# Optimization experiments

Hardware: AMD Instinct MI355X
Metric: run time of the kernel (lower is better)

Reference implementation:

```python
import jax, jax.numpy as jnp
import numpy as np

SHIFT = 1  # fixed shift_direction (module draws +/-1 at random; we pin +1)

def setup_inputs() -> dict:
    key = jax.random.key(0)
    kx, kw = jax.random.split(key)
    x = jax.random.normal(kx, (1024, 256, 7, 7), dtype=jnp.float32)
    W = jax.random.normal(kw, (128, 3, 3, 512), dtype=jnp.float32)
    return {"x": x, "W": W}

def _fwd(x, W):
    B = x.shape[0]
    t = x.reshape(B, 256, 7, 7)
    # unfold((3,1), padding=(1,0)) along H: t[b,c,k,h,w] = x_pad[b,c,h+k-1,w]
    xp = jnp.pad(t, ((0, 0), (0, 0), (1, 1), (0, 0)))
    t = jnp.stack([xp[:, :, k:k + 7, :] for k in range(3)], axis=2)  # (B,256,3,7,7)
    t = t.reshape(B, 2, 128, 3, 7, 7).transpose(0, 2, 3, 4, 1, 5)   # (B,128,3,7,2,7)
    t = t.reshape(B, 128, 3, 14, 7)
    t = jnp.roll(t, SHIFT, axis=3)
    t = t.reshape(B, 128, 3, 7, 2, 7).sum(axis=4)                   # (B,128,3,7,7)
    t = t.transpose(0, 1, 3, 2, 4)                                  # (B,128,7,3,7)
    t = jnp.roll(t, SHIFT, axis=4)
    # second unfold((3,1), padding=(1,0)) along W dim: gather 3 shifted slices
    tp = jnp.pad(t, ((0, 0), (0, 0), (0, 0), (0, 0), (1, 1)))
    t3 = jnp.stack([tp[..., k2:k2 + 7] for k2 in range(3)], axis=-1)  # (B,128,7,3,7,3) = (m,l,n,j,o,k)
    out = jnp.einsum('mlnjok,ljki->mnoi', t3, W)                     # (B,7,7,512)
    return out.transpose(0, 3, 1, 2)                                 # (B,512,7,7)

def reference(x, W):
    return _fwd(x, W)
```

## Files before the change

kernel.cpp:

```cpp
#include <hip/hip_runtime.h>

typedef __attribute__((ext_vector_type(8)))  __bf16 bvec8;
typedef __attribute__((ext_vector_type(4)))  __bf16 bvec4;
typedef __attribute__((ext_vector_type(16))) float  fvec16;
typedef __attribute__((ext_vector_type(8)))  short  svec8;

__global__ __launch_bounds__(256) void pack_w(const float* __restrict__ W,
                                              __bf16* __restrict__ Wp) {
    int u = blockIdx.x * 256 + threadIdx.x;
    if (u >= 73728) return;
    int lane = u & 63;
    int f    = (u >> 6) & 3;
    int wd   = (u >> 8) & 7;
    int t    = u >> 11;
    int am = f & 1, h = f >> 1;
    int i  = (wd << 6) + (am << 5) + (lane & 31);
    int K0 = ((2 * t + h) << 4) + ((lane >> 5) << 3);
    bvec8 o;
#pragma unroll
    for (int e = 0; e < 8; ++e) {
        int K  = K0 + e;
        int jk = K >> 7;
        int l  = K & 127;
        int j  = (jk * 11) >> 5;
        int k  = jk - 3 * j;
        o[e] = (__bf16)W[((l * 9 + j * 3 + k) << 9) + i];
    }
    *(bvec8*)&Wp[(size_t)u * 8] = o;
}

__global__ __launch_bounds__(512, 2) void conv_mfma(
    const float* __restrict__ x, const __bf16* __restrict__ Wp,
    float* __restrict__ out)
{
    __shared__ __align__(16) char smem[65024];
    __bf16* xs = (__bf16*)smem;
    __bf16* ys = (__bf16*)(smem + 25088);

    const int tid  = threadIdx.x;
    const int lane = tid & 63;
    const int l31  = lane & 31;
    const int ls5  = lane >> 5;
    const int wd   = tid >> 6;
    const int b0   = blockIdx.x * 2;

    const float* xb  = x + (size_t)b0 * 12544;
    const char*  WpB = (const char*)Wp;
    const int wbase  = wd * 4096 + lane * 16;

    bvec8 aE[2][2], aO[2][2];
#pragma unroll
    for (int am = 0; am < 2; ++am)
#pragma unroll
        for (int h = 0; h < 2; ++h) {
            aE[am][h] = *(const bvec8*)(WpB + wbase + ((h * 2 + am) << 10));
            aO[am][h] = *(const bvec8*)(WpB + 32768 + wbase + ((h * 2 + am) << 10));
        }

    for (int bb = 0; bb < 2; ++bb) {
        for (int it = 0; it < 7; ++it) {
            int e4 = it * 512 + tid;
            if (e4 < 3136) {
                const float4 v = ((const float4*)(xb + bb * 12544))[e4];
                bvec4 pk = { (__bf16)v.x, (__bf16)v.y, (__bf16)v.z, (__bf16)v.w };
                *(bvec4*)&xs[e4 * 4] = pk;
            }
        }
        __syncthreads();
        for (int it = 0; it < 3; ++it) {
            int up = it * 512 + tid;
            if (up < 1248) {
                int row  = up >> 4;
                int useg = up & 15;
                int l0   = useg * 8;
                bvec8 ov;
                if (row == 77) {
                    ov = __builtin_bit_cast(bvec8, (svec8)0);
                } else if (row < 63) {
                    int t = row / 7, w = row - t * 7;
                    int tb = t + 5; if (tb >= 7) tb -= 7;
                    int cB = tb * 7 + w;
                    bool mA = (t >= 1) && (t <= 7);
                    int cA = mA ? (t - 1) * 7 + w : 0;
#pragma unroll
                    for (int d = 0; d < 8; ++d) {
                        float fa = mA ? (float)xs[(l0 + d) * 49 + cA] : 0.f;
                        float fb = (float)xs[(128 + l0 + d) * 49 + cB];
                        ov[d] = (__bf16)(fa + fb);
                    }
                } else if (row < 70) {
                    int w = row - 63;
#pragma unroll
                    for (int d = 0; d < 8; ++d) ov[d] = xs[(l0 + d) * 49 + w];
                } else {
                    int w = row - 70;
#pragma unroll
                    for (int d = 0; d < 8; ++d) ov[d] = xs[(l0 + d) * 49 + 7 + w];
                }
                *(bvec8*)&ys[((bb * 78 + row) << 7) + ((useg ^ (row & 15)) << 3)] = ov;
            }
        }
        __syncthreads();
    }

    int nq[2], oo[2];
#pragma unroll
    for (int sn = 0; sn < 2; ++sn) {
        int s = sn * 32 + l31;
        int sc = (s < 49) ? s : 48;
        nq[sn] = sc / 7;
        oo[sn] = sc - nq[sn] * 7;
    }

    fvec16 acc[2][2][2];
#pragma unroll
    for (int am = 0; am < 2; ++am)
#pragma unroll
        for (int sn = 0; sn < 2; ++sn)
#pragma unroll
            for (int bb = 0; bb < 2; ++bb)
#pragma unroll
                for (int r = 0; r < 16; ++r) acc[am][sn][bb][r] = 0.f;

#define GEO(JK, ROWE, RX) {                                                   \
        int j_ = ((JK) * 11) >> 5; int k_ = (JK) - 3 * j_;                    \
        _Pragma("unroll")                                                     \
        for (int sn_ = 0; sn_ < 2; ++sn_) {                                   \
            int tw_ = oo[sn_] + k_ + 5; int w_ = tw_ >= 7 ? tw_ - 7 : tw_;    \
            int row_ = (nq[sn_] + j_) * 7 + w_;                               \
            if (nq[sn_] == 1 && j_ == 0) row_ = 63 + w_;                      \
            if (nq[sn_] == 0 && j_ == 2) row_ = 70 + w_;                      \
            if ((k_ == 0 && oo[sn_] == 0) || (k_ == 2 && oo[sn_] == 6))       \
                row_ = 77;                                                    \
            ROWE[sn_] = row_ << 7; RX[sn_] = row_ & 15; } }

#define READF(DST, P, ROWE, RX) {                                             \
        _Pragma("unroll")                                                     \
        for (int sn_ = 0; sn_ < 2; ++sn_)                                     \
        _Pragma("unroll")                                                     \
        for (int h_ = 0; h_ < 2; ++h_) {                                      \
            int u_ = ((P) * 4 + h_ * 2 + ls5) ^ RX[sn_];                      \
            DST[sn_][0][h_] = *(const bvec8*)&ys[ROWE[sn_] + (u_ << 3)];      \
            DST[sn_][1][h_] = *(const bvec8*)&ys[9984 + ROWE[sn_] + (u_ << 3)]; } }

#define MFMA16(AW, BF) {                                                      \
        __builtin_amdgcn_s_setprio(1);                                        \
        _Pragma("unroll")                                                     \
        for (int h_ = 0; h_ < 2; ++h_)                                        \
        _Pragma("unroll")                                                     \
        for (int am_ = 0; am_ < 2; ++am_)                                     \
        _Pragma("unroll")                                                     \
        for (int sn_ = 0; sn_ < 2; ++sn_)                                     \
        _Pragma("unroll")                                                     \
        for (int bb_ = 0; bb_ < 2; ++bb_)                                     \
            acc[am_][sn_][bb_] = __builtin_amdgcn_mfma_f32_32x32x16_bf16(     \
                AW[am_][h_], BF[sn_][bb_][h_], acc[am_][sn_][bb_], 0, 0, 0);  \
        __builtin_amdgcn_s_setprio(0); }

#define PREFW(AW, TT) {                                                       \
        const char* gp_ = WpB + ((size_t)(TT) << 15) + wbase;                 \
        _Pragma("unroll")                                                     \
        for (int am_ = 0; am_ < 2; ++am_)                                     \
        _Pragma("unroll")                                                     \
        for (int h_ = 0; h_ < 2; ++h_)                                        \
            AW[am_][h_] = *(const bvec8*)(gp_ + ((h_ * 2 + am_) << 10)); }

    int rowE[2], rx[2], rowEn[2], rxn[2];
    GEO(0, rowE, rx);
    bvec8 bfA[2][2][2], bfB[2][2][2];
    READF(bfA, 0, rowE, rx);

    for (int jk = 0; jk < 9; ++jk) {
        const int t0 = jk * 4;
        READF(bfB, 1, rowE, rx);
        MFMA16(aE, bfA);
        PREFW(aE, t0 + 2);
        READF(bfA, 2, rowE, rx);
        MFMA16(aO, bfB);
        PREFW(aO, t0 + 3);
        { int jn = jk < 8 ? jk + 1 : 8; GEO(jn, rowEn, rxn); }
        READF(bfB, 3, rowE, rx);
        MFMA16(aE, bfA);
        if (jk < 8) PREFW(aE, t0 + 4);
        READF(bfA, 0, rowEn, rxn);
        MFMA16(aO, bfB);
        if (jk < 8) PREFW(aO, t0 + 5);
#pragma unroll
        for (int sn = 0; sn < 2; ++sn) { rowE[sn] = rowEn[sn]; rx[sn] = rxn[sn]; }
    }

#undef GEO
#undef READF
#undef MFMA16
#undef PREFW

#pragma unroll
    for (int am = 0; am < 2; ++am) {
        const int i0 = wd * 64 + am * 32 + 4 * ls5;
#pragma unroll
        for (int sn = 0; sn < 2; ++sn) {
            if (sn == 1 && l31 >= 17) continue;
            const int s = sn * 32 + l31;
#pragma unroll
            for (int bb = 0; bb < 2; ++bb) {
                const size_t ob = (size_t)(b0 + bb) * 25088;
#pragma unroll
                for (int r = 0; r < 16; ++r) {
                    int i = i0 + (r & 3) + 8 * (r >> 2);
                    out[ob + (size_t)i * 49 + s] = acc[am][sn][bb][r];
                }
            }
        }
    }
}

extern "C" void kernel_launch(void* const* d_in, const int* in_sizes, int n_in,
                              void* d_out, int out_size, void* d_ws, size_t ws_size,
                              hipStream_t stream) {
    const float* x = (const float*)d_in[0];
    const float* W = (const float*)d_in[1];
    float* out = (float*)d_out;
    __bf16* Wp = (__bf16*)d_ws;
    (void)in_sizes; (void)n_in; (void)out_size; (void)ws_size;

    hipLaunchKernelGGL(pack_w, dim3(288), dim3(256), 0, stream, W, Wp);
    hipLaunchKernelGGL(conv_mfma, dim3(512), dim3(512), 0, stream, x, Wp, out);
}
```

Baseline: 92.60 us.

## Double block to 1024 threads with each wave owning 32 output channels

```diff
diff --git a/kernel.cpp b/kernel.cpp
--- a/kernel.cpp
+++ b/kernel.cpp
@@ -10,11 +10,10 @@
     int u = blockIdx.x * 256 + threadIdx.x;
     if (u >= 73728) return;
     int lane = u & 63;
-    int f    = (u >> 6) & 3;
-    int wd   = (u >> 8) & 7;
+    int h    = (u >> 6) & 1;
+    int it   = (u >> 7) & 15;
     int t    = u >> 11;
-    int am = f & 1, h = f >> 1;
-    int i  = (wd << 6) + (am << 5) + (lane & 31);
+    int i  = (it << 5) + (lane & 31);
     int K0 = ((2 * t + h) << 4) + ((lane >> 5) << 3);
     bvec8 o;
 #pragma unroll
@@ -29,7 +28,7 @@
     *(bvec8*)&Wp[(size_t)u * 8] = o;
 }
 
-__global__ __launch_bounds__(512, 2) void conv_mfma(
+__global__ __launch_bounds__(1024, 4) void conv_mfma(
     const float* __restrict__ x, const __bf16* __restrict__ Wp,
     float* __restrict__ out)
 {
@@ -46,20 +45,18 @@
 
     const float* xb  = x + (size_t)b0 * 12544;
     const char*  WpB = (const char*)Wp;
-    const int wbase  = wd * 4096 + lane * 16;
+    const int wbase  = wd * 2048 + lane * 16;
 
-    bvec8 aE[2][2], aO[2][2];
+    bvec8 aE[2], aO[2];
 #pragma unroll
-    for (int am = 0; am < 2; ++am)
-#pragma unroll
-        for (int h = 0; h < 2; ++h) {
-            aE[am][h] = *(const bvec8*)(WpB + wbase + ((h * 2 + am) << 10));
-            aO[am][h] = *(const bvec8*)(WpB + 32768 + wbase + ((h * 2 + am) << 10));
-        }
+    for (int h = 0; h < 2; ++h) {
+        aE[h] = *(const bvec8*)(WpB + wbase + (h << 10));
+        aO[h] = *(const bvec8*)(WpB + 32768 + wbase + (h << 10));
+    }
 
     for (int bb = 0; bb < 2; ++bb) {
-        for (int it = 0; it < 7; ++it) {
-            int e4 = it * 512 + tid;
+        for (int it = 0; it < 4; ++it) {
+            int e4 = it * 1024 + tid;
             if (e4 < 3136) {
                 const float4 v = ((const float4*)(xb + bb * 12544))[e4];
                 bvec4 pk = { (__bf16)v.x, (__bf16)v.y, (__bf16)v.z, (__bf16)v.w };
@@ -67,8 +64,8 @@
             }
         }
         __syncthreads();
-        for (int it = 0; it < 3; ++it) {
-            int up = it * 512 + tid;
+        for (int it = 0; it < 2; ++it) {
+            int up = it * 1024 + tid;
             if (up < 1248) {
                 int row  = up >> 4;
                 int useg = up & 15;
@@ -112,15 +109,13 @@
         oo[sn] = sc - nq[sn] * 7;
     }
 
-    fvec16 acc[2][2][2];
+    fvec16 acc[2][2];
 #pragma unroll
-    for (int am = 0; am < 2; ++am)
+    for (int sn = 0; sn < 2; ++sn)
 #pragma unroll
-        for (int sn = 0; sn < 2; ++sn)
+        for (int bb = 0; bb < 2; ++bb)
 #pragma unroll
-            for (int bb = 0; bb < 2; ++bb)
-#pragma unroll
-                for (int r = 0; r < 16; ++r) acc[am][sn][bb][r] = 0.f;
+            for (int r = 0; r < 16; ++r) acc[sn][bb][r] = 0.f;
 
 #define GEO(JK, ROWE, RX) {                                                   \
         int j_ = ((JK) * 11) >> 5; int k_ = (JK) - 3 * j_;                    \
@@ -134,81 +129,56 @@
                 row_ = 77;                                                    \
             ROWE[sn_] = row_ << 7; RX[sn_] = row_ & 15; } }
 
-#define READF(DST, P, ROWE, RX) {                                             \
-        _Pragma("unroll")                                                     \
-        for (int sn_ = 0; sn_ < 2; ++sn_)                                     \
+#define STEP(P, AW, TNEXT, DOPF) {                                            \
+        bvec8 bf[2][2];                                                       \
+        __builtin_amdgcn_s_setprio(1);                                        \
         _Pragma("unroll")                                                     \
         for (int h_ = 0; h_ < 2; ++h_) {                                      \
-            int u_ = ((P) * 4 + h_ * 2 + ls5) ^ RX[sn_];                      \
-            DST[sn_][0][h_] = *(const bvec8*)&ys[ROWE[sn_] + (u_ << 3)];      \
-            DST[sn_][1][h_] = *(const bvec8*)&ys[9984 + ROWE[sn_] + (u_ << 3)]; } }
+            _Pragma("unroll")                                                 \
+            for (int sn_ = 0; sn_ < 2; ++sn_) {                               \
+                int u_ = ((P) * 4 + h_ * 2 + ls5) ^ rx[sn_];                  \
+                bf[sn_][0] = *(const bvec8*)&ys[rowE[sn_] + (u_ << 3)];       \
+                bf[sn_][1] = *(const bvec8*)&ys[9984 + rowE[sn_] + (u_ << 3)];\
+            }                                                                 \
+            _Pragma("unroll")                                                 \
+            for (int sn_ = 0; sn_ < 2; ++sn_)                                 \
+            _Pragma("unroll")                                                 \
+            for (int bb_ = 0; bb_ < 2; ++bb_)                                 \
+                acc[sn_][bb_] = __builtin_amdgcn_mfma_f32_32x32x16_bf16(      \
+                    AW[h_], bf[sn_][bb_], acc[sn_][bb_], 0, 0, 0);            \
+        }                                                                     \
+        __builtin_amdgcn_s_setprio(0);                                        \
+        if (DOPF) {                                                           \
+            const char* gp_ = WpB + ((size_t)(TNEXT) << 15) + wbase;          \
+            AW[0] = *(const bvec8*)(gp_);                                     \
+            AW[1] = *(const bvec8*)(gp_ + 1024);                              \
+        } }
 
-#define MFMA16(AW, BF) {                                                      \
-        __builtin_amdgcn_s_setprio(1);                                        \
-        _Pragma("unroll")                                                     \
-        for (int h_ = 0; h_ < 2; ++h_)                                        \
-        _Pragma("unroll")                                                     \
-        for (int am_ = 0; am_ < 2; ++am_)                                     \
-        _Pragma("unroll")                                                     \
-        for (int sn_ = 0; sn_ < 2; ++sn_)                                     \
-        _Pragma("unroll")                                                     \
-        for (int bb_ = 0; bb_ < 2; ++bb_)                                     \
-            acc[am_][sn_][bb_] = __builtin_amdgcn_mfma_f32_32x32x16_bf16(     \
-                AW[am_][h_], BF[sn_][bb_][h_], acc[am_][sn_][bb_], 0, 0, 0);  \
-        __builtin_amdgcn_s_setprio(0); }
-
-#define PREFW(AW, TT) {                                                       \
-        const char* gp_ = WpB + ((size_t)(TT) << 15) + wbase;                 \
-        _Pragma("unroll")                                                     \
-        for (int am_ = 0; am_ < 2; ++am_)                                     \
-        _Pragma("unroll")                                                     \
-        for (int h_ = 0; h_ < 2; ++h_)                                        \
-            AW[am_][h_] = *(const bvec8*)(gp_ + ((h_ * 2 + am_) << 10)); }
-
-    int rowE[2], rx[2], rowEn[2], rxn[2];
-    GEO(0, rowE, rx);
-    bvec8 bfA[2][2][2], bfB[2][2][2];
-    READF(bfA, 0, rowE, rx);
-
+    int rowE[2], rx[2];
     for (int jk = 0; jk < 9; ++jk) {
         const int t0 = jk * 4;
-        READF(bfB, 1, rowE, rx);
-        MFMA16(aE, bfA);
-        PREFW(aE, t0 + 2);
-        READF(bfA, 2, rowE, rx);
-        MFMA16(aO, bfB);
-        PREFW(aO, t0 + 3);
-        { int jn = jk < 8 ? jk + 1 : 8; GEO(jn, rowEn, rxn); }
-        READF(bfB, 3, rowE, rx);
-        MFMA16(aE, bfA);
-        if (jk < 8) PREFW(aE, t0 + 4);
-        READF(bfA, 0, rowEn, rxn);
-        MFMA16(aO, bfB);
-        if (jk < 8) PREFW(aO, t0 + 5);
-#pragma unroll
-        for (int sn = 0; sn < 2; ++sn) { rowE[sn] = rowEn[sn]; rx[sn] = rxn[sn]; }
+        GEO(jk, rowE, rx);
+        STEP(0, aE, t0 + 2, true)
+        STEP(1, aO, t0 + 3, true)
+        STEP(2, aE, t0 + 4, (jk < 8))
+        STEP(3, aO, t0 + 5, (jk < 8))
     }
 
 #undef GEO
-#undef READF
-#undef MFMA16
-#undef PREFW
+#undef STEP
 
+    const int i0 = wd * 32 + 4 * ls5;
 #pragma unroll
-    for (int am = 0; am < 2; ++am) {
-        const int i0 = wd * 64 + am * 32 + 4 * ls5;
+    for (int sn = 0; sn < 2; ++sn) {
+        if (sn == 1 && l31 >= 17) continue;
+        const int s = sn * 32 + l31;
 #pragma unroll
-        for (int sn = 0; sn < 2; ++sn) {
-            if (sn == 1 && l31 >= 17) continue;
-            const int s = sn * 32 + l31;
+        for (int bb = 0; bb < 2; ++bb) {
+            const size_t ob = (size_t)(b0 + bb) * 25088;
 #pragma unroll
-            for (int bb = 0; bb < 2; ++bb) {
-                const size_t ob = (size_t)(b0 + bb) * 25088;
-#pragma unroll
-                for (int r = 0; r < 16; ++r) {
-                    int i = i0 + (r & 3) + 8 * (r >> 2);
-                    out[ob + (size_t)i * 49 + s] = acc[am][sn][bb][r];
-                }
+            for (int r = 0; r < 16; ++r) {
+                int i = i0 + (r & 3) + 8 * (r >> 2);
+                out[ob + (size_t)i * 49 + s] = acc[sn][bb][r];
             }
         }
     }
@@ -224,5 +194,5 @@
     (void)in_sizes; (void)n_in; (void)out_size; (void)ws_size;
 
     hipLaunchKernelGGL(pack_w, dim3(288), dim3(256), 0, stream, W, Wp);
-    hipLaunchKernelGGL(conv_mfma, dim3(512), dim3(512), 0, stream, x, Wp, out);
+    hipLaunchKernelGGL(conv_mfma, dim3(512), dim3(1024), 0, stream, x, Wp, out);
 }
```

Result: faster. 90.08 us (-2.7%).

## Split batch pair across 16 waves, one batch item per wave group

Applied to the files above, without the earlier changes.

```diff
diff --git a/kernel.cpp b/kernel.cpp
--- a/kernel.cpp
+++ b/kernel.cpp
@@ -29,7 +29,7 @@
     *(bvec8*)&Wp[(size_t)u * 8] = o;
 }
 
-__global__ __launch_bounds__(512, 2) void conv_mfma(
+__global__ __launch_bounds__(1024, 4) void conv_mfma(
     const float* __restrict__ x, const __bf16* __restrict__ Wp,
     float* __restrict__ out)
 {
@@ -42,11 +42,14 @@
     const int l31  = lane & 31;
     const int ls5  = lane >> 5;
     const int wd   = tid >> 6;
+    const int wi   = wd & 7;
+    const int bbw  = wd >> 3;
     const int b0   = blockIdx.x * 2;
 
     const float* xb  = x + (size_t)b0 * 12544;
     const char*  WpB = (const char*)Wp;
-    const int wbase  = wd * 4096 + lane * 16;
+    const int wbase  = wi * 4096 + lane * 16;
+    const int ysb    = bbw * 9984;
 
     bvec8 aE[2][2], aO[2][2];
 #pragma unroll
@@ -58,8 +61,8 @@
         }
 
     for (int bb = 0; bb < 2; ++bb) {
-        for (int it = 0; it < 7; ++it) {
-            int e4 = it * 512 + tid;
+        for (int it = 0; it < 4; ++it) {
+            int e4 = it * 1024 + tid;
             if (e4 < 3136) {
                 const float4 v = ((const float4*)(xb + bb * 12544))[e4];
                 bvec4 pk = { (__bf16)v.x, (__bf16)v.y, (__bf16)v.z, (__bf16)v.w };
@@ -67,8 +70,8 @@
             }
         }
         __syncthreads();
-        for (int it = 0; it < 3; ++it) {
-            int up = it * 512 + tid;
+        for (int it = 0; it < 2; ++it) {
+            int up = it * 1024 + tid;
             if (up < 1248) {
                 int row  = up >> 4;
                 int useg = up & 15;
@@ -112,15 +115,13 @@
         oo[sn] = sc - nq[sn] * 7;
     }
 
-    fvec16 acc[2][2][2];
+    fvec16 acc[2][2];
 #pragma unroll
     for (int am = 0; am < 2; ++am)
 #pragma unroll
         for (int sn = 0; sn < 2; ++sn)
 #pragma unroll
-            for (int bb = 0; bb < 2; ++bb)
-#pragma unroll
-                for (int r = 0; r < 16; ++r) acc[am][sn][bb][r] = 0.f;
+            for (int r = 0; r < 16; ++r) acc[am][sn][r] = 0.f;
 
 #define GEO(JK, ROWE, RX) {                                                   \
         int j_ = ((JK) * 11) >> 5; int k_ = (JK) - 3 * j_;                    \
@@ -140,10 +141,9 @@
         _Pragma("unroll")                                                     \
         for (int h_ = 0; h_ < 2; ++h_) {                                      \
             int u_ = ((P) * 4 + h_ * 2 + ls5) ^ RX[sn_];                      \
-            DST[sn_][0][h_] = *(const bvec8*)&ys[ROWE[sn_] + (u_ << 3)];      \
-            DST[sn_][1][h_] = *(const bvec8*)&ys[9984 + ROWE[sn_] + (u_ << 3)]; } }
-
-#define MFMA16(AW, BF) {                                                      \
+            DST[sn_][h_] = *(const bvec8*)&ys[ysb + ROWE[sn_] + (u_ << 3)]; } }
+
+#define MFMA8(AW, BF) {                                                       \
         __builtin_amdgcn_s_setprio(1);                                        \
         _Pragma("unroll")                                                     \
         for (int h_ = 0; h_ < 2; ++h_)                                        \
@@ -151,10 +151,8 @@
         for (int am_ = 0; am_ < 2; ++am_)                                     \
         _Pragma("unroll")                                                     \
         for (int sn_ = 0; sn_ < 2; ++sn_)                                     \
-        _Pragma("unroll")                                                     \
-        for (int bb_ = 0; bb_ < 2; ++bb_)                                     \
-            acc[am_][sn_][bb_] = __builtin_amdgcn_mfma_f32_32x32x16_bf16(     \
-                AW[am_][h_], BF[sn_][bb_][h_], acc[am_][sn_][bb_], 0, 0, 0);  \
+            acc[am_][sn_] = __builtin_amdgcn_mfma_f32_32x32x16_bf16(          \
+                AW[am_][h_], BF[sn_][h_], acc[am_][sn_], 0, 0, 0);            \
         __builtin_amdgcn_s_setprio(0); }
 
 #define PREFW(AW, TT) {                                                       \
@@ -167,23 +165,23 @@
 
     int rowE[2], rx[2], rowEn[2], rxn[2];
     GEO(0, rowE, rx);
-    bvec8 bfA[2][2][2], bfB[2][2][2];
+    bvec8 bfA[2][2], bfB[2][2];
     READF(bfA, 0, rowE, rx);
 
     for (int jk = 0; jk < 9; ++jk) {
         const int t0 = jk * 4;
         READF(bfB, 1, rowE, rx);
-        MFMA16(aE, bfA);
+        MFMA8(aE, bfA);
         PREFW(aE, t0 + 2);
         READF(bfA, 2, rowE, rx);
-        MFMA16(aO, bfB);
+        MFMA8(aO, bfB);
         PREFW(aO, t0 + 3);
         { int jn = jk < 8 ? jk + 1 : 8; GEO(jn, rowEn, rxn); }
         READF(bfB, 3, rowE, rx);
-        MFMA16(aE, bfA);
+        MFMA8(aE, bfA);
         if (jk < 8) PREFW(aE, t0 + 4);
         READF(bfA, 0, rowEn, rxn);
-        MFMA16(aO, bfB);
+        MFMA8(aO, bfB);
         if (jk < 8) PREFW(aO, t0 + 5);
 #pragma unroll
         for (int sn = 0; sn < 2; ++sn) { rowE[sn] = rowEn[sn]; rx[sn] = rxn[sn]; }
@@ -191,24 +189,21 @@
 
 #undef GEO
 #undef READF
-#undef MFMA16
+#undef MFMA8
 #undef PREFW
 
+    const size_t ob = (size_t)(b0 + bbw) * 25088;
 #pragma unroll
     for (int am = 0; am < 2; ++am) {
-        const int i0 = wd * 64 + am * 32 + 4 * ls5;
+        const int i0 = wi * 64 + am * 32 + 4 * ls5;
 #pragma unroll
         for (int sn = 0; sn < 2; ++sn) {
             if (sn == 1 && l31 >= 17) continue;
             const int s = sn * 32 + l31;
 #pragma unroll
-            for (int bb = 0; bb < 2; ++bb) {
-                const size_t ob = (size_t)(b0 + bb) * 25088;
-#pragma unroll
-                for (int r = 0; r < 16; ++r) {
-                    int i = i0 + (r & 3) + 8 * (r >> 2);
-                    out[ob + (size_t)i * 49 + s] = acc[am][sn][bb][r];
-                }
+            for (int r = 0; r < 16; ++r) {
+                int i = i0 + (r & 3) + 8 * (r >> 2);
+                out[ob + (size_t)i * 49 + s] = acc[am][sn][r];
             }
         }
     }
@@ -224,5 +219,5 @@
     (void)in_sizes; (void)n_in; (void)out_size; (void)ws_size;
 
     hipLaunchKernelGGL(pack_w, dim3(288), dim3(256), 0, stream, W, Wp);
-    hipLaunchKernelGGL(conv_mfma, dim3(512), dim3(512), 0, stream, x, Wp, out);
+    hipLaunchKernelGGL(conv_mfma, dim3(512), dim3(1024), 0, stream, x, Wp, out);
 }
```

Result: slower. 194.7 us (+110.2%).
